# Performance work log

Measured on AMD Instinct MI355X. Metric: run time of the kernel, lower is better.

The kernel has to match this reference:

```python
import jax, jax.numpy as jnp
import numpy as np

N, E, H_DIM, HEADS = 20000, 640000, 128, 8
HD = H_DIM // HEADS  # head_dim = 16


def setup_inputs() -> dict:
    key = jax.random.key(0)
    ks = jax.random.split(key, 12)
    def xavier(k, shape):
        fan_in, fan_out = shape[0], shape[1]
        lim = jnp.sqrt(6.0 / (fan_in + fan_out))
        return jax.random.uniform(k, shape, jnp.float32, -lim, lim)
    return {
        "x": jax.random.normal(ks[0], (N, H_DIM), jnp.float32),
        "edge_index": jax.random.randint(ks[1], (2, E), 0, N, jnp.int64 if jax.config.x64_enabled else jnp.int32),
        "edge_attr": jax.random.normal(ks[2], (E, H_DIM), jnp.float32),
        "WQ": xavier(ks[3], (H_DIM, H_DIM)),
        "WK": xavier(ks[4], (H_DIM, H_DIM)),
        "WV": xavier(ks[5], (H_DIM, H_DIM)),
        "WE": xavier(ks[6], (H_DIM, H_DIM)),
        "Wout": xavier(ks[7], (H_DIM, H_DIM)),
        "bout": jnp.zeros((H_DIM,), jnp.float32),
        "gn_w": jnp.ones((H_DIM,), jnp.float32),
        "gn_b": jnp.zeros((H_DIM,), jnp.float32),
        "gn_ms": jnp.ones((H_DIM,), jnp.float32),
    }


def reference(x, edge_index, edge_attr, WQ, WK, WV, WE, Wout, bout, gn_w, gn_b, gn_ms):
    n = x.shape[0]
    src, dst = edge_index[0], edge_index[1]  # PyG: row=source j, col=target i

    q = (x @ WQ).reshape(n, HEADS, HD)
    k = (x @ WK).reshape(n, HEADS, HD)
    v = (x @ WV).reshape(n, HEADS, HD)
    e = (edge_attr @ WE).reshape(-1, HEADS, HD)

    # per-edge attention score [E, HEADS]
    score = jnp.sum(q[dst] * (k[src] + e), axis=-1) / jnp.sqrt(jnp.asarray(HD, x.dtype))

    # scatter-softmax over edges grouped by destination node
    seg_max = jax.ops.segment_max(score, dst, num_segments=n)  # [N, HEADS]
    seg_max = jnp.where(jnp.isfinite(seg_max), seg_max, 0.0)
    ex = jnp.exp(score - seg_max[dst])
    denom = jax.ops.segment_sum(ex, dst, num_segments=n)
    alpha = ex / (denom[dst] + 1e-16)  # [E, HEADS]

    # weighted scatter-add aggregation
    msg = alpha[..., None] * (v[src] + e)  # [E, HEADS, HD]
    out = jax.ops.segment_sum(msg, dst, num_segments=n).reshape(n, H_DIM)

    out = out @ Wout + bout
    h = out + x  # residual (DropPath is identity in eval)

    # GraphNorm with batch=None -> single-graph normalization
    mean = jnp.mean(h, axis=0)
    o = h - mean * gn_ms
    var = jnp.mean(o * o, axis=0)
    o = gn_w * o / jnp.sqrt(var + 1e-5) + gn_b

    return jax.nn.gelu(o, approximate=False)
```

## Files before the change

### kernel.cpp

```cpp
#include <hip/hip_runtime.h>

using u16 = unsigned short;
using u32 = unsigned int;
typedef float f32x4 __attribute__((ext_vector_type(4)));
typedef float f32x2 __attribute__((ext_vector_type(2)));
typedef short s16x8 __attribute__((ext_vector_type(8)));
typedef u32   u32x2 __attribute__((ext_vector_type(2)));
typedef u32   u32x4 __attribute__((ext_vector_type(4)));

__device__ __forceinline__ u16 f2bf(float f) {
  u32 u = __float_as_uint(f);
  u += 0x7fffu + ((u >> 16) & 1u);
  return (u16)(u >> 16);
}
__device__ __forceinline__ float bf2f(u16 h) {
  return __uint_as_float(((u32)h) << 16);
}

__global__ void ROEN_Final_33526514713351_kernel() {}


__global__ void roen_zero(int* __restrict__ count, int N, float* __restrict__ dbg) {
  int i = blockIdx.x * 256 + threadIdx.x;
  if (i == 0) dbg[0] = 1000.0f;
  if (i < N) count[i] = 0;
}

__global__ void roen_hist(const int* __restrict__ ei, int E, int* __restrict__ count,
                          int* __restrict__ rank, float* __restrict__ dbg) {
  int i = blockIdx.x * 256 + threadIdx.x;
  if (i == 0) dbg[1] = 1001.0f;
  if (i < E) rank[i] = atomicAdd(&count[ei[E + i]], 1);
}

__global__ __launch_bounds__(1024) void roen_scan(const int* __restrict__ count, int N,
                                                  int* __restrict__ off,
                                                  float* __restrict__ dbg) {
  __shared__ int wsum[16];
  __shared__ int carrys;
  int tid = threadIdx.x, lane = tid & 63, wv = tid >> 6;
  if (tid == 0) { dbg[2] = 1002.0f; carrys = 0; }
  __syncthreads();
  for (int base = 0; base < N; base += 1024) {
    int i = base + tid;
    int v = (i < N) ? count[i] : 0;
    int x = v;
#pragma unroll
    for (int s = 1; s < 64; s <<= 1) {
      int t = __shfl_up(x, s);
      if (lane >= s) x += t;
    }
    if (lane == 63) wsum[wv] = x;
    __syncthreads();
    if (wv == 0 && lane < 16) {
      int y = wsum[lane];
#pragma unroll
      for (int s = 1; s < 16; s <<= 1) {
        int t = __shfl_up(y, s);
        if (lane >= s) y += t;
      }
      wsum[lane] = y;
    }
    __syncthreads();
    int wbase = (wv == 0) ? 0 : wsum[wv - 1];
    int incl = x + wbase + carrys;
    if (i < N) off[i] = incl - v;
    __syncthreads();
    if (tid == 1023) carrys = incl;
    __syncthreads();
  }
  if (tid == 0) off[N] = carrys;
}

__global__ void roen_scatter(const int* __restrict__ ei, const int* __restrict__ off,
                             const int* __restrict__ rank, int E,
                             int* __restrict__ inv, int* __restrict__ srcS,
                             int* __restrict__ dstS, float* __restrict__ dbg) {
  int i = blockIdx.x * 256 + threadIdx.x;
  if (i == 0) dbg[3] = 1003.0f;
  if (i < E) {
    int d = ei[E + i];
    int p = off[d] + rank[i];
    inv[i] = p;
    srcS[p] = ei[i];
    dstS[p] = d;
  }
}

__global__ void roen_prep_w(const float* __restrict__ W0, const float* __restrict__ W1,
                            const float* __restrict__ W2, const float* __restrict__ W3,
                            const float* __restrict__ W4, u16* __restrict__ Wt,
                            float* __restrict__ dbg) {
  int w = blockIdx.x;
  if (w == 0 && threadIdx.x == 0) dbg[4] = 1004.0f;
  const float* W = (w == 0) ? W0 : (w == 1) ? W1 : (w == 2) ? W2 : (w == 3) ? W3 : W4;
  for (int idx = threadIdx.x; idx < 16384; idx += 256) {
    int n = idx >> 7, k = idx & 127;
    Wt[w * 16384 + idx] = f2bf(W[k * 128 + n]);
  }
}

__global__ __launch_bounds__(256) void roen_gemm_qkv(const float* __restrict__ x,
                                                     const u16* __restrict__ Wt,
                                                     u16* __restrict__ qb, u16* __restrict__ kb,
                                                     u32* __restrict__ vb2, int M,
                                                     float* __restrict__ dbg) {
  __shared__ u16 As[64 * 128];
  const int tid = threadIdx.x;
  if (blockIdx.x == 0 && tid == 0) dbg[5] = 1005.0f;
  const long brow = (long)blockIdx.x * 64;

  {
    f32x4 tmp[8];
#pragma unroll
    for (int j = 0; j < 8; ++j) {
      int idx = j * 256 + tid;
      int row = idx >> 5;
      int c4 = (idx & 31) * 4;
      long grow = brow + row;
      f32x4 a = {0.f, 0.f, 0.f, 0.f};
      if (grow < M) a = *(const f32x4*)(x + grow * 128 + c4);
      tmp[j] = a;
    }
#pragma unroll
    for (int j = 0; j < 8; ++j) {
      int idx = j * 256 + tid;
      int row = idx >> 5;
      int c4 = (idx & 31) * 4;
      u32 lo = ((u32)f2bf(tmp[j][1]) << 16) | (u32)f2bf(tmp[j][0]);
      u32 hi = ((u32)f2bf(tmp[j][3]) << 16) | (u32)f2bf(tmp[j][2]);
      int byte = (row * 256 + c4 * 2) ^ ((row & 7) << 4);
      u32x2 val; val[0] = lo; val[1] = hi;
      *(u32x2*)((char*)As + byte) = val;
    }
  }
  __syncthreads();

  const int wave = tid >> 6, lane = tid & 63;
  const int wc = wave * 32;
  const int lr = lane & 15, lg = lane >> 4;

  s16x8 af[4][4];
#pragma unroll
  for (int ks = 0; ks < 4; ++ks) {
    int kb2 = (ks * 32 + lg * 8) * 2;
#pragma unroll
    for (int mt = 0; mt < 4; ++mt) {
      int row = mt * 16 + lr;
      int byte = (row * 256 + kb2) ^ ((row & 7) << 4);
      af[ks][mt] = *(const s16x8*)((const char*)As + byte);
    }
  }

  for (int w = 0; w < 3; ++w) {
    s16x8 bfr[4][2];
#pragma unroll
    for (int ks = 0; ks < 4; ++ks)
#pragma unroll
      for (int nt = 0; nt < 2; ++nt)
        bfr[ks][nt] = *(const s16x8*)(Wt + w * 16384 + (wc + nt * 16 + lr) * 128 + ks * 32 + lg * 8);

    f32x4 acc[4][2];
    for (int mt = 0; mt < 4; ++mt)
      for (int nt = 0; nt < 2; ++nt) acc[mt][nt] = {0.f, 0.f, 0.f, 0.f};

#pragma unroll
    for (int ks = 0; ks < 4; ++ks)
      for (int mt = 0; mt < 4; ++mt)
        for (int nt = 0; nt < 2; ++nt)
          acc[mt][nt] = __builtin_amdgcn_mfma_f32_16x16x32_bf16(af[ks][mt], bfr[ks][nt], acc[mt][nt], 0, 0, 0);

    if (w == 2) {
      for (int mt = 0; mt < 4; ++mt) {
        for (int r = 0; r < 4; ++r) {
          long row = brow + mt * 16 + lg * 4 + r;
          if (row < M) {
            u32 val = (u32)f2bf(acc[mt][0][r]) | ((u32)f2bf(acc[mt][1][r]) << 16);
            vb2[row * 64 + wave * 16 + lr] = val;
          }
        }
      }
    } else {
      u16* C = (w == 0) ? qb : kb;
      for (int mt = 0; mt < 4; ++mt) {
        for (int nt = 0; nt < 2; ++nt) {
          int col = wc + nt * 16 + lr;
          for (int r = 0; r < 4; ++r) {
            long row = brow + mt * 16 + lg * 4 + r;
            if (row < M) C[row * 128 + col] = f2bf(acc[mt][nt][r]);
          }
        }
      }
    }
  }
}

__global__ __launch_bounds__(256) void roen_gemm_e(const float* __restrict__ ea,
                                                   const u16* __restrict__ WtE,
                                                   const int* __restrict__ inv,
                                                   u32* __restrict__ eS2, int E,
                                                   float* __restrict__ dbg) {
  __shared__ u16 As[64 * 128];
  __shared__ int invv[64];
  const int tid = threadIdx.x;
  if (blockIdx.x == 0 && tid == 0) dbg[6] = 1006.0f;
  const long brow = (long)blockIdx.x * 64;

  if (tid < 64) {
    long pos = brow + tid;
    invv[tid] = (pos < E) ? inv[pos] : -1;
  }

  {
    f32x4 tmp[8];
#pragma unroll
    for (int j = 0; j < 8; ++j) {
      int idx = j * 256 + tid;
      int row = idx >> 5;
      int c4 = (idx & 31) * 4;
      long grow = brow + row;
      f32x4 a = {0.f, 0.f, 0.f, 0.f};
      if (grow < E) a = *(const f32x4*)(ea + grow * 128 + c4);
      tmp[j] = a;
    }
#pragma unroll
    for (int j = 0; j < 8; ++j) {
      int idx = j * 256 + tid;
      int row = idx >> 5;
      int c4 = (idx & 31) * 4;
      u32 lo = ((u32)f2bf(tmp[j][1]) << 16) | (u32)f2bf(tmp[j][0]);
      u32 hi = ((u32)f2bf(tmp[j][3]) << 16) | (u32)f2bf(tmp[j][2]);
      int byte = (row * 256 + c4 * 2) ^ ((row & 7) << 4);
      u32x2 val; val[0] = lo; val[1] = hi;
      *(u32x2*)((char*)As + byte) = val;
    }
  }
  __syncthreads();

  const int wave = tid >> 6, lane = tid & 63;
  const int wc = wave * 32;
  const int lr = lane & 15, lg = lane >> 4;

  s16x8 bfr[4][2];
#pragma unroll
  for (int ks = 0; ks < 4; ++ks)
#pragma unroll
    for (int nt = 0; nt < 2; ++nt)
      bfr[ks][nt] = *(const s16x8*)(WtE + (wc + nt * 16 + lr) * 128 + ks * 32 + lg * 8);

  f32x4 acc[4][2];
  for (int mt = 0; mt < 4; ++mt)
    for (int nt = 0; nt < 2; ++nt) acc[mt][nt] = {0.f, 0.f, 0.f, 0.f};

  for (int ks = 0; ks < 4; ++ks) {
    int kb2 = (ks * 32 + lg * 8) * 2;
    s16x8 af[4];
    for (int mt = 0; mt < 4; ++mt) {
      int row = mt * 16 + lr;
      int byte = (row * 256 + kb2) ^ ((row & 7) << 4);
      af[mt] = *(const s16x8*)((const char*)As + byte);
    }
    for (int mt = 0; mt < 4; ++mt)
      for (int nt = 0; nt < 2; ++nt)
        acc[mt][nt] = __builtin_amdgcn_mfma_f32_16x16x32_bf16(af[mt], bfr[ks][nt], acc[mt][nt], 0, 0, 0);
  }

  for (int mt = 0; mt < 4; ++mt) {
    for (int r = 0; r < 4; ++r) {
      int row = mt * 16 + lg * 4 + r;
      int op = invv[row];
      if (op >= 0) {
        u32 val = (u32)f2bf(acc[mt][0][r]) | ((u32)f2bf(acc[mt][1][r]) << 16);
        eS2[(long)op * 64 + wave * 16 + lr] = val;
      }
    }
  }
}

__global__ __launch_bounds__(256) void roen_score(const int* __restrict__ srcS,
                                                  const int* __restrict__ dstS,
                                                  const u16* __restrict__ qb,
                                                  const u16* __restrict__ kb,
                                                  const u32* __restrict__ eS2,
                                                  float* __restrict__ wS, int E,
                                                  float* __restrict__ dbg) {
  long gid = (long)blockIdx.x * 256 + threadIdx.x;
  if (gid == 0) dbg[9] = 1009.0f;
  long pos = gid >> 3;
  int h = (int)(gid & 7);
  if (pos >= E) return;
  int dst = dstS[pos], src = srcS[pos];
  const s16x8* qp = (const s16x8*)(qb + (long)dst * 128 + h * 16);
  const s16x8* kp = (const s16x8*)(kb + (long)src * 128 + h * 16);
  const u32x4* ep = (const u32x4*)(eS2 + (long)pos * 64 + (h >> 1) * 16);
  const int sh = (h & 1) * 16;
  float acc = 0.f;
#pragma unroll
  for (int c = 0; c < 2; ++c) {
    s16x8 qv = qp[c], kv = kp[c];
    u32x4 ea_ = ep[c * 2], eb_ = ep[c * 2 + 1];
#pragma unroll
    for (int j = 0; j < 4; ++j) {
      float e0 = bf2f((u16)(ea_[j] >> sh));
      float e1 = bf2f((u16)(eb_[j] >> sh));
      acc += bf2f((u16)qv[j]) * (bf2f((u16)kv[j]) + e0);
      acc += bf2f((u16)qv[j + 4]) * (bf2f((u16)kv[j + 4]) + e1);
    }
  }
  wS[pos * 8 + h] = __expf(fminf(acc * 0.25f, 80.f));
}

__global__ __launch_bounds__(256) void roen_node_agg(const int* __restrict__ off,
                                                     const int* __restrict__ srcS,
                                                     const u32* __restrict__ eS2,
                                                     const u32* __restrict__ vb2,
                                                     const float* __restrict__ wS,
                                                     float* __restrict__ outat, int N,
                                                     float* __restrict__ dbg) {
  int wave = threadIdx.x >> 6;
  int lane = threadIdx.x & 63;
  int node = blockIdx.x * 4 + wave;
  if (node == 0 && lane == 0) dbg[10] = 1010.0f;
  if (node >= N) return;
  int beg = off[node], end = off[node + 1];

  const int dA = 32 * (lane >> 4) + (lane & 15);
  const int dB = dA + 16;
  const int hA = dA >> 4;
  float accA = 0.f, accB = 0.f, dsA = 0.f, dsB = 0.f;

  int pos = beg;
  for (; pos + 4 <= end; pos += 4) {
    int s0 = srcS[pos], s1 = srcS[pos + 1], s2 = srcS[pos + 2], s3 = srcS[pos + 3];
    f32x2 w0 = *(const f32x2*)(wS + (long)(pos + 0) * 8 + hA);
    f32x2 w1 = *(const f32x2*)(wS + (long)(pos + 1) * 8 + hA);
    f32x2 w2 = *(const f32x2*)(wS + (long)(pos + 2) * 8 + hA);
    f32x2 w3 = *(const f32x2*)(wS + (long)(pos + 3) * 8 + hA);
    u32 e0 = eS2[(long)(pos + 0) * 64 + lane];
    u32 e1 = eS2[(long)(pos + 1) * 64 + lane];
    u32 e2 = eS2[(long)(pos + 2) * 64 + lane];
    u32 e3 = eS2[(long)(pos + 3) * 64 + lane];
    u32 v0 = vb2[(long)s0 * 64 + lane];
    u32 v1 = vb2[(long)s1 * 64 + lane];
    u32 v2 = vb2[(long)s2 * 64 + lane];
    u32 v3 = vb2[(long)s3 * 64 + lane];
    accA += w0[0] * (bf2f((u16)v0) + bf2f((u16)e0));
    accB += w0[1] * (bf2f((u16)(v0 >> 16)) + bf2f((u16)(e0 >> 16)));
    accA += w1[0] * (bf2f((u16)v1) + bf2f((u16)e1));
    accB += w1[1] * (bf2f((u16)(v1 >> 16)) + bf2f((u16)(e1 >> 16)));
    accA += w2[0] * (bf2f((u16)v2) + bf2f((u16)e2));
    accB += w2[1] * (bf2f((u16)(v2 >> 16)) + bf2f((u16)(e2 >> 16)));
    accA += w3[0] * (bf2f((u16)v3) + bf2f((u16)e3));
    accB += w3[1] * (bf2f((u16)(v3 >> 16)) + bf2f((u16)(e3 >> 16)));
    dsA += w0[0] + w1[0] + w2[0] + w3[0];
    dsB += w0[1] + w1[1] + w2[1] + w3[1];
  }
  for (; pos < end; ++pos) {
    f32x2 w = *(const f32x2*)(wS + (long)pos * 8 + hA);
    u32 ev = eS2[(long)pos * 64 + lane];
    int src = srcS[pos];
    u32 vv = vb2[(long)src * 64 + lane];
    accA += w[0] * (bf2f((u16)vv) + bf2f((u16)ev));
    accB += w[1] * (bf2f((u16)(vv >> 16)) + bf2f((u16)(ev >> 16)));
    dsA += w[0]; dsB += w[1];
  }
  outat[(long)node * 128 + dA] = accA / (dsA + 1e-16f);
  outat[(long)node * 128 + dB] = accB / (dsB + 1e-16f);
}

__global__ __launch_bounds__(256) void roen_gemm_out(const float* __restrict__ A,
                                                     const u16* __restrict__ Wt,
                                                     const float* __restrict__ x,
                                                     const float* __restrict__ bo,
                                                     float* __restrict__ h,
                                                     float* __restrict__ psum,
                                                     float* __restrict__ psumsq, int M,
                                                     float* __restrict__ dbg) {
  __shared__ u16 As[64 * 128];
  const int tid = threadIdx.x;
  if (blockIdx.x == 0 && tid == 0) dbg[11] = 1011.0f;
  const long brow = (long)blockIdx.x * 64;

  {
    f32x4 tmp[8];
#pragma unroll
    for (int j = 0; j < 8; ++j) {
      int idx = j * 256 + tid;
      int row = idx >> 5;
      int c4 = (idx & 31) * 4;
      long grow = brow + row;
      f32x4 a = {0.f, 0.f, 0.f, 0.f};
      if (grow < M) a = *(const f32x4*)(A + grow * 128 + c4);
      tmp[j] = a;
    }
#pragma unroll
    for (int j = 0; j < 8; ++j) {
      int idx = j * 256 + tid;
      int row = idx >> 5;
      int c4 = (idx & 31) * 4;
      u32 lo = ((u32)f2bf(tmp[j][1]) << 16) | (u32)f2bf(tmp[j][0]);
      u32 hi = ((u32)f2bf(tmp[j][3]) << 16) | (u32)f2bf(tmp[j][2]);
      int byte = (row * 256 + c4 * 2) ^ ((row & 7) << 4);
      u32x2 val; val[0] = lo; val[1] = hi;
      *(u32x2*)((char*)As + byte) = val;
    }
  }

  const int wave = tid >> 6, lane = tid & 63;
  const int wc = wave * 32;
  const int lr = lane & 15, lg = lane >> 4;

  s16x8 bfr[4][2];
#pragma unroll
  for (int ks = 0; ks < 4; ++ks)
#pragma unroll
    for (int nt = 0; nt < 2; ++nt)
      bfr[ks][nt] = *(const s16x8*)(Wt + (wc + nt * 16 + lr) * 128 + ks * 32 + lg * 8);

  __syncthreads();

  f32x4 acc[4][2];
  for (int mt = 0; mt < 4; ++mt)
    for (int nt = 0; nt < 2; ++nt) acc[mt][nt] = {0.f, 0.f, 0.f, 0.f};

  for (int ks = 0; ks < 4; ++ks) {
    int kb2 = (ks * 32 + lg * 8) * 2;
    s16x8 af[4];
    for (int mt = 0; mt < 4; ++mt) {
      int row = mt * 16 + lr;
      int byte = (row * 256 + kb2) ^ ((row & 7) << 4);
      af[mt] = *(const s16x8*)((const char*)As + byte);
    }
    for (int mt = 0; mt < 4; ++mt)
      for (int nt = 0; nt < 2; ++nt)
        acc[mt][nt] = __builtin_amdgcn_mfma_f32_16x16x32_bf16(af[mt], bfr[ks][nt], acc[mt][nt], 0, 0, 0);
  }

  float b0 = bo[wc + lr];
  float b1 = bo[wc + 16 + lr];
  float cs[2] = {0.f, 0.f}, cs2[2] = {0.f, 0.f};
  for (int mt = 0; mt < 4; ++mt) {
    for (int nt = 0; nt < 2; ++nt) {
      int col = wc + nt * 16 + lr;
      float bb = (nt == 0) ? b0 : b1;
      for (int r = 0; r < 4; ++r) {
        long row = brow + mt * 16 + lg * 4 + r;
        if (row < M) {
          long idx = row * 128 + col;
          float val = acc[mt][nt][r] + bb + x[idx];
          h[idx] = val;
          cs[nt] += val;
          cs2[nt] += val * val;
        }
      }
    }
  }
#pragma unroll
  for (int nt = 0; nt < 2; ++nt) {
    cs[nt] += __shfl_xor(cs[nt], 16);
    cs[nt] += __shfl_xor(cs[nt], 32);
    cs2[nt] += __shfl_xor(cs2[nt], 16);
    cs2[nt] += __shfl_xor(cs2[nt], 32);
  }
  if (lg == 0) {
    int col0 = wc + lr;
    psum[(long)blockIdx.x * 128 + col0] = cs[0];
    psumsq[(long)blockIdx.x * 128 + col0] = cs2[0];
    psum[(long)blockIdx.x * 128 + col0 + 16] = cs[1];
    psumsq[(long)blockIdx.x * 128 + col0 + 16] = cs2[1];
  }
}

__global__ void roen_stats(const float* __restrict__ psum, const float* __restrict__ psumsq,
                           const float* __restrict__ gnw, const float* __restrict__ gnb,
                           const float* __restrict__ gnms, float* __restrict__ Ac,
                           float* __restrict__ Bc, int nb, int N, float* __restrict__ dbg) {
  int d = threadIdx.x;
  if (d == 0) dbg[13] = 1013.0f;
  float s = 0.f, s2 = 0.f;
  for (int i = 0; i < nb; ++i) {
    s += psum[(long)i * 128 + d];
    s2 += psumsq[(long)i * 128 + d];
  }
  float mean = s / (float)N;
  float mm = mean * gnms[d];
  float var = s2 / (float)N - 2.f * mm * mean + mm * mm;
  float scale = gnw[d] * rsqrtf(var + 1e-5f);
  Ac[d] = scale;
  Bc[d] = gnb[d] - mm * scale;
}

__global__ __launch_bounds__(256) void roen_final(const float* __restrict__ h,
                                                  const float* __restrict__ Ac,
                                                  const float* __restrict__ Bc,
                                                  float* __restrict__ out, long total) {
  long i = (long)blockIdx.x * 256 + threadIdx.x;
  if (i >= total) return;
  int d = (int)(i & 127);
  float v = h[i] * Ac[d] + Bc[d];
  out[i] = 0.5f * v * (1.f + erff(v * 0.70710678f));
}

extern "C" void kernel_launch(void* const* d_in, const int* in_sizes, int n_in,
                              void* d_out, int out_size, void* d_ws, size_t ws_size,
                              hipStream_t stream) {
  const float* x   = (const float*)d_in[0];
  const int*   ei  = (const int*)d_in[1];
  const float* ea  = (const float*)d_in[2];
  const float* WQ  = (const float*)d_in[3];
  const float* WK  = (const float*)d_in[4];
  const float* WV  = (const float*)d_in[5];
  const float* WE  = (const float*)d_in[6];
  const float* Wo  = (const float*)d_in[7];
  const float* bo  = (const float*)d_in[8];
  const float* gnw = (const float*)d_in[9];
  const float* gnb = (const float*)d_in[10];
  const float* gnms= (const float*)d_in[11];
  float* out = (float*)d_out;
  float* dbg = (float*)d_out;

  const int N = in_sizes[0] / 128;
  const int E = in_sizes[1] / 2;
  const int gN = (N + 63) / 64;

  char* base = (char*)d_ws;
  size_t cur = 0;
  auto alloc = [&](size_t bytes) -> char* {
    char* r = base + cur;
    cur = (cur + bytes + 255) & ~(size_t)255;
    return r;
  };
  u16*   wt     = (u16*)alloc(5 * 16384 * sizeof(u16));
  u16*   qb     = (u16*)alloc((size_t)N * 128 * sizeof(u16));
  u16*   kb     = (u16*)alloc((size_t)N * 128 * sizeof(u16));
  u32*   vb2    = (u32*)alloc((size_t)N * 64 * sizeof(u32));
  float* wS     = (float*)alloc((size_t)E * 8 * sizeof(float));
  int*   count  = (int*)alloc((size_t)N * sizeof(int));
  int*   offar  = (int*)alloc((size_t)(N + 1) * sizeof(int));
  int*   rank   = (int*)alloc((size_t)E * sizeof(int));
  int*   invar  = (int*)alloc((size_t)E * sizeof(int));
  int*   srcS   = (int*)alloc((size_t)E * sizeof(int));
  int*   dstS   = (int*)alloc((size_t)E * sizeof(int));
  float* outat  = (float*)alloc((size_t)N * 128 * sizeof(float));
  float* psum   = (float*)alloc((size_t)gN * 128 * sizeof(float));
  float* psumsq = (float*)alloc((size_t)gN * 128 * sizeof(float));
  float* Ac     = (float*)alloc(128 * sizeof(float));
  float* Bc     = (float*)alloc(128 * sizeof(float));
  u32*   eS2    = (u32*)alloc((size_t)E * 64 * sizeof(u32));
  float* hbuf   = (float*)eS2;

  roen_zero<<<(N + 255) / 256, 256, 0, stream>>>(count, N, dbg);
  roen_hist<<<(E + 255) / 256, 256, 0, stream>>>(ei, E, count, rank, dbg);
  roen_scan<<<1, 1024, 0, stream>>>(count, N, offar, dbg);
  roen_scatter<<<(E + 255) / 256, 256, 0, stream>>>(ei, offar, rank, E, invar, srcS, dstS, dbg);
  roen_prep_w<<<5, 256, 0, stream>>>(WQ, WK, WV, WE, Wo, wt, dbg);

  roen_gemm_qkv<<<gN, 256, 0, stream>>>(x, wt, qb, kb, vb2, N, dbg);
  roen_gemm_e<<<(E + 63) / 64, 256, 0, stream>>>(ea, wt + 3 * 16384, invar, eS2, E, dbg);

  roen_score<<<(int)(((long)E * 8 + 255) / 256), 256, 0, stream>>>(srcS, dstS, qb, kb, eS2, wS, E, dbg);
  roen_node_agg<<<(N + 3) / 4, 256, 0, stream>>>(offar, srcS, eS2, vb2, wS, outat, N, dbg);

  roen_gemm_out<<<gN, 256, 0, stream>>>(outat, wt + 4 * 16384, x, bo, hbuf, psum, psumsq, N, dbg);
  roen_stats<<<1, 128, 0, stream>>>(psum, psumsq, gnw, gnb, gnms, Ac, Bc, gN, N, dbg);
  roen_final<<<(int)(((long)N * 128 + 255) / 256), 256, 0, stream>>>(hbuf, Ac, Bc, out, (long)N * 128);
}
```

Before: 415.3 us.

## Fuse edge score computation into per-node aggregation and merge zero into weight prep

The separate per-edge score kernel is folded into the per-destination aggregation kernel. Each wave now computes the exp-scores for 8 edges at a time, loading q once per node, and broadcasts them across lanes with shuffles. This removes the E×8 float score buffer write and read-back, and with it the dstS array and its scatter write. The count-zeroing kernel is also merged into the weight-prep launch to save one launch. In exchange, each wave reads the edge features twice per edge and does extra shuffle and predicated work when a node has fewer edges than a multiple of 8.

```diff
diff --git a/kernel.cpp b/kernel.cpp
--- a/kernel.cpp
+++ b/kernel.cpp
@@ -20,10 +20,23 @@
 __global__ void ROEN_Final_33526514713351_kernel() {}
 
 
-__global__ void roen_zero(int* __restrict__ count, int N, float* __restrict__ dbg) {
-  int i = blockIdx.x * 256 + threadIdx.x;
-  if (i == 0) dbg[0] = 1000.0f;
-  if (i < N) count[i] = 0;
+__global__ void roen_prep_w(const float* __restrict__ W0, const float* __restrict__ W1,
+                            const float* __restrict__ W2, const float* __restrict__ W3,
+                            const float* __restrict__ W4, u16* __restrict__ Wt,
+                            int* __restrict__ count, int N, float* __restrict__ dbg) {
+  int b = blockIdx.x;
+  if (b < 5) {
+    if (b == 0 && threadIdx.x == 0) dbg[4] = 1004.0f;
+    const float* W = (b == 0) ? W0 : (b == 1) ? W1 : (b == 2) ? W2 : (b == 3) ? W3 : W4;
+    for (int idx = threadIdx.x; idx < 16384; idx += 256) {
+      int n = idx >> 7, k = idx & 127;
+      Wt[b * 16384 + idx] = f2bf(W[k * 128 + n]);
+    }
+  } else {
+    int i = (b - 5) * 256 + threadIdx.x;
+    if (i == 0) dbg[0] = 1000.0f;
+    if (i < N) count[i] = 0;
+  }
 }
 
 __global__ void roen_hist(const int* __restrict__ ei, int E, int* __restrict__ count,
@@ -75,7 +88,7 @@
 __global__ void roen_scatter(const int* __restrict__ ei, const int* __restrict__ off,
                              const int* __restrict__ rank, int E,
                              int* __restrict__ inv, int* __restrict__ srcS,
-                             int* __restrict__ dstS, float* __restrict__ dbg) {
+                             float* __restrict__ dbg) {
   int i = blockIdx.x * 256 + threadIdx.x;
   if (i == 0) dbg[3] = 1003.0f;
   if (i < E) {
@@ -83,20 +96,6 @@
     int p = off[d] + rank[i];
     inv[i] = p;
     srcS[p] = ei[i];
-    dstS[p] = d;
-  }
-}
-
-__global__ void roen_prep_w(const float* __restrict__ W0, const float* __restrict__ W1,
-                            const float* __restrict__ W2, const float* __restrict__ W3,
-                            const float* __restrict__ W4, u16* __restrict__ Wt,
-                            float* __restrict__ dbg) {
-  int w = blockIdx.x;
-  if (w == 0 && threadIdx.x == 0) dbg[4] = 1004.0f;
-  const float* W = (w == 0) ? W0 : (w == 1) ? W1 : (w == 2) ? W2 : (w == 3) ? W3 : W4;
-  for (int idx = threadIdx.x; idx < 16384; idx += 256) {
-    int n = idx >> 7, k = idx & 127;
-    Wt[w * 16384 + idx] = f2bf(W[k * 128 + n]);
   }
 }
 
@@ -277,92 +276,70 @@
   }
 }
 
-__global__ __launch_bounds__(256) void roen_score(const int* __restrict__ srcS,
-                                                  const int* __restrict__ dstS,
-                                                  const u16* __restrict__ qb,
-                                                  const u16* __restrict__ kb,
-                                                  const u32* __restrict__ eS2,
-                                                  float* __restrict__ wS, int E,
-                                                  float* __restrict__ dbg) {
-  long gid = (long)blockIdx.x * 256 + threadIdx.x;
-  if (gid == 0) dbg[9] = 1009.0f;
-  long pos = gid >> 3;
-  int h = (int)(gid & 7);
-  if (pos >= E) return;
-  int dst = dstS[pos], src = srcS[pos];
-  const s16x8* qp = (const s16x8*)(qb + (long)dst * 128 + h * 16);
-  const s16x8* kp = (const s16x8*)(kb + (long)src * 128 + h * 16);
-  const u32x4* ep = (const u32x4*)(eS2 + (long)pos * 64 + (h >> 1) * 16);
-  const int sh = (h & 1) * 16;
-  float acc = 0.f;
-#pragma unroll
-  for (int c = 0; c < 2; ++c) {
-    s16x8 qv = qp[c], kv = kp[c];
-    u32x4 ea_ = ep[c * 2], eb_ = ep[c * 2 + 1];
-#pragma unroll
-    for (int j = 0; j < 4; ++j) {
-      float e0 = bf2f((u16)(ea_[j] >> sh));
-      float e1 = bf2f((u16)(eb_[j] >> sh));
-      acc += bf2f((u16)qv[j]) * (bf2f((u16)kv[j]) + e0);
-      acc += bf2f((u16)qv[j + 4]) * (bf2f((u16)kv[j + 4]) + e1);
-    }
-  }
-  wS[pos * 8 + h] = __expf(fminf(acc * 0.25f, 80.f));
-}
-
-__global__ __launch_bounds__(256) void roen_node_agg(const int* __restrict__ off,
-                                                     const int* __restrict__ srcS,
-                                                     const u32* __restrict__ eS2,
-                                                     const u32* __restrict__ vb2,
-                                                     const float* __restrict__ wS,
-                                                     float* __restrict__ outat, int N,
-                                                     float* __restrict__ dbg) {
+__global__ __launch_bounds__(256) void roen_agg(const int* __restrict__ off,
+                                                const int* __restrict__ srcS,
+                                                const u16* __restrict__ qb,
+                                                const u16* __restrict__ kb,
+                                                const u32* __restrict__ eS2,
+                                                const u32* __restrict__ vb2,
+                                                float* __restrict__ outat, int N,
+                                                float* __restrict__ dbg) {
   int wave = threadIdx.x >> 6;
   int lane = threadIdx.x & 63;
   int node = blockIdx.x * 4 + wave;
-  if (node == 0 && lane == 0) dbg[10] = 1010.0f;
+  if (node == 0 && lane == 0) dbg[9] = 1009.0f;
   if (node >= N) return;
   int beg = off[node], end = off[node + 1];
+
+  const int eidx = lane >> 3;
+  const int sh = lane & 7;
+  const int g16 = (sh >> 1) * 16;
+  const int shv = (sh & 1) * 16;
+  const s16x8* qp = (const s16x8*)(qb + (long)node * 128 + sh * 16);
+  s16x8 q0 = qp[0], q1 = qp[1];
 
   const int dA = 32 * (lane >> 4) + (lane & 15);
   const int dB = dA + 16;
   const int hA = dA >> 4;
   float accA = 0.f, accB = 0.f, dsA = 0.f, dsB = 0.f;
 
-  int pos = beg;
-  for (; pos + 4 <= end; pos += 4) {
-    int s0 = srcS[pos], s1 = srcS[pos + 1], s2 = srcS[pos + 2], s3 = srcS[pos + 3];
-    f32x2 w0 = *(const f32x2*)(wS + (long)(pos + 0) * 8 + hA);
-    f32x2 w1 = *(const f32x2*)(wS + (long)(pos + 1) * 8 + hA);
-    f32x2 w2 = *(const f32x2*)(wS + (long)(pos + 2) * 8 + hA);
-    f32x2 w3 = *(const f32x2*)(wS + (long)(pos + 3) * 8 + hA);
-    u32 e0 = eS2[(long)(pos + 0) * 64 + lane];
-    u32 e1 = eS2[(long)(pos + 1) * 64 + lane];
-    u32 e2 = eS2[(long)(pos + 2) * 64 + lane];
-    u32 e3 = eS2[(long)(pos + 3) * 64 + lane];
-    u32 v0 = vb2[(long)s0 * 64 + lane];
-    u32 v1 = vb2[(long)s1 * 64 + lane];
-    u32 v2 = vb2[(long)s2 * 64 + lane];
-    u32 v3 = vb2[(long)s3 * 64 + lane];
-    accA += w0[0] * (bf2f((u16)v0) + bf2f((u16)e0));
-    accB += w0[1] * (bf2f((u16)(v0 >> 16)) + bf2f((u16)(e0 >> 16)));
-    accA += w1[0] * (bf2f((u16)v1) + bf2f((u16)e1));
-    accB += w1[1] * (bf2f((u16)(v1 >> 16)) + bf2f((u16)(e1 >> 16)));
-    accA += w2[0] * (bf2f((u16)v2) + bf2f((u16)e2));
-    accB += w2[1] * (bf2f((u16)(v2 >> 16)) + bf2f((u16)(e2 >> 16)));
-    accA += w3[0] * (bf2f((u16)v3) + bf2f((u16)e3));
-    accB += w3[1] * (bf2f((u16)(v3 >> 16)) + bf2f((u16)(e3 >> 16)));
-    dsA += w0[0] + w1[0] + w2[0] + w3[0];
-    dsB += w0[1] + w1[1] + w2[1] + w3[1];
-  }
-  for (; pos < end; ++pos) {
-    f32x2 w = *(const f32x2*)(wS + (long)pos * 8 + hA);
-    u32 ev = eS2[(long)pos * 64 + lane];
-    int src = srcS[pos];
-    u32 vv = vb2[(long)src * 64 + lane];
-    accA += w[0] * (bf2f((u16)vv) + bf2f((u16)ev));
-    accB += w[1] * (bf2f((u16)(vv >> 16)) + bf2f((u16)(ev >> 16)));
-    dsA += w[0]; dsB += w[1];
+  for (int cbeg = beg; cbeg < end; cbeg += 8) {
+    long spos = cbeg + eidx;
+    float w = 0.f;
+    if (spos < end) {
+      int src = srcS[spos];
+      const s16x8* kp = (const s16x8*)(kb + (long)src * 128 + sh * 16);
+      s16x8 k0 = kp[0], k1 = kp[1];
+      const u32x4* ep = (const u32x4*)(eS2 + spos * 64 + g16);
+      u32x4 e0 = ep[0], e1 = ep[1], e2 = ep[2], e3 = ep[3];
+      float acc = 0.f;
+#pragma unroll
+      for (int j = 0; j < 4; ++j) {
+        acc += bf2f((u16)q0[j])     * (bf2f((u16)k0[j])     + bf2f((u16)(e0[j] >> shv)));
+        acc += bf2f((u16)q0[j + 4]) * (bf2f((u16)k0[j + 4]) + bf2f((u16)(e1[j] >> shv)));
+        acc += bf2f((u16)q1[j])     * (bf2f((u16)k1[j])     + bf2f((u16)(e2[j] >> shv)));
+        acc += bf2f((u16)q1[j + 4]) * (bf2f((u16)k1[j + 4]) + bf2f((u16)(e3[j] >> shv)));
+      }
+      w = __expf(fminf(acc * 0.25f, 80.f));
+    }
+
+    u32 evs[8], vvs[8];
+#pragma unroll
+    for (int i = 0; i < 8; ++i) {
+      long pos = cbeg + i;
+      bool ok = pos < end;
+      int src = ok ? srcS[pos] : 0;
+      evs[i] = ok ? eS2[pos * 64 + lane] : 0u;
+      vvs[i] = ok ? vb2[(long)src * 64 + lane] : 0u;
+    }
+#pragma unroll
+    for (int i = 0; i < 8; ++i) {
+      float wA = __shfl(w, i * 8 + hA);
+      float wB = __shfl(w, i * 8 + hA + 1);
+      accA += wA * (bf2f((u16)evs[i]) + bf2f((u16)vvs[i]));
+      accB += wB * (bf2f((u16)(evs[i] >> 16)) + bf2f((u16)(vvs[i] >> 16)));
+      dsA += wA; dsB += wB;
+    }
   }
   outat[(long)node * 128 + dA] = accA / (dsA + 1e-16f);
   outat[(long)node * 128 + dB] = accB / (dsB + 1e-16f);
@@ -534,13 +511,11 @@
   u16*   qb     = (u16*)alloc((size_t)N * 128 * sizeof(u16));
   u16*   kb     = (u16*)alloc((size_t)N * 128 * sizeof(u16));
   u32*   vb2    = (u32*)alloc((size_t)N * 64 * sizeof(u32));
-  float* wS     = (float*)alloc((size_t)E * 8 * sizeof(float));
   int*   count  = (int*)alloc((size_t)N * sizeof(int));
   int*   offar  = (int*)alloc((size_t)(N + 1) * sizeof(int));
   int*   rank   = (int*)alloc((size_t)E * sizeof(int));
   int*   invar  = (int*)alloc((size_t)E * sizeof(int));
   int*   srcS   = (int*)alloc((size_t)E * sizeof(int));
-  int*   dstS   = (int*)alloc((size_t)E * sizeof(int));
   float* outat  = (float*)alloc((size_t)N * 128 * sizeof(float));
   float* psum   = (float*)alloc((size_t)gN * 128 * sizeof(float));
   float* psumsq = (float*)alloc((size_t)gN * 128 * sizeof(float));
@@ -549,17 +524,15 @@
   u32*   eS2    = (u32*)alloc((size_t)E * 64 * sizeof(u32));
   float* hbuf   = (float*)eS2;
 
-  roen_zero<<<(N + 255) / 256, 256, 0, stream>>>(count, N, dbg);
+  roen_prep_w<<<5 + (N + 255) / 256, 256, 0, stream>>>(WQ, WK, WV, WE, Wo, wt, count, N, dbg);
   roen_hist<<<(E + 255) / 256, 256, 0, stream>>>(ei, E, count, rank, dbg);
   roen_scan<<<1, 1024, 0, stream>>>(count, N, offar, dbg);
-  roen_scatter<<<(E + 255) / 256, 256, 0, stream>>>(ei, offar, rank, E, invar, srcS, dstS, dbg);
-  roen_prep_w<<<5, 256, 0, stream>>>(WQ, WK, WV, WE, Wo, wt, dbg);
+  roen_scatter<<<(E + 255) / 256, 256, 0, stream>>>(ei, offar, rank, E, invar, srcS, dbg);
 
   roen_gemm_qkv<<<gN, 256, 0, stream>>>(x, wt, qb, kb, vb2, N, dbg);
   roen_gemm_e<<<(E + 63) / 64, 256, 0, stream>>>(ea, wt + 3 * 16384, invar, eS2, E, dbg);
 
-  roen_score<<<(int)(((long)E * 8 + 255) / 256), 256, 0, stream>>>(srcS, dstS, qb, kb, eS2, wS, E, dbg);
-  roen_node_agg<<<(N + 3) / 4, 256, 0, stream>>>(offar, srcS, eS2, vb2, wS, outat, N, dbg);
+  roen_agg<<<(N + 3) / 4, 256, 0, stream>>>(offar, srcS, qb, kb, eS2, vb2, outat, N, dbg);
 
   roen_gemm_out<<<gN, 256, 0, stream>>>(outat, wt + 4 * 16384, x, bo, hbuf, psum, psumsq, N, dbg);
   roen_stats<<<1, 128, 0, stream>>>(psum, psumsq, gnw, gnb, gnms, Ac, Bc, gN, N, dbg);
```

Measured after the change: 437.0 us. 5.2% more time.
